# Kernel tuning notes

Measured on AMD Instinct MI355X. Metric: run time of the kernel, lower is better.

Reference implementation:

```python
import jax, jax.numpy as jnp
import numpy as np

C = 128      # c_in
H = 4        # no_heads
DH = 32      # c_hidden // no_heads (per-head dim)
INF = 1e9
EPS = 1e-5


def setup_inputs() -> dict:
    key = jax.random.key(0)
    ks = jax.random.split(key, 10)
    B, I, J = 1, 384, 384
    x = jax.random.normal(ks[0], (B, I, J, C), dtype=jnp.float32)
    mask = jnp.ones((B, I, J), dtype=jnp.float32)
    s = 0.02
    return {
        "x": x,
        "mask": mask,
        "ln_w": jnp.ones((C,), jnp.float32),
        "ln_b": jnp.zeros((C,), jnp.float32),
        "w_tri": jax.random.normal(ks[1], (C, H), jnp.float32) * s,   # bias=False
        "wq": jax.random.normal(ks[2], (C, H * DH), jnp.float32) * s,
        "wk": jax.random.normal(ks[3], (C, H * DH), jnp.float32) * s,
        "wv": jax.random.normal(ks[4], (C, H * DH), jnp.float32) * s,
        "wg": jax.random.normal(ks[5], (C, H * DH), jnp.float32) * s,
        "bg": jnp.zeros((H * DH,), jnp.float32),
        "wo": jax.random.normal(ks[6], (H * DH, C), jnp.float32) * s,
        "bo": jnp.zeros((C,), jnp.float32),
    }


def reference(x, mask, ln_w, ln_b, w_tri, wq, wk, wv, wg, bg, wo, bo):
    # starting=True: attend along rows (J axis), no transpose.
    B, I, J, _ = x.shape
    # LayerNorm over channel dim
    mu = jnp.mean(x, axis=-1, keepdims=True)
    var = jnp.mean(jnp.square(x - mu), axis=-1, keepdims=True)
    xn = (x - mu) * jax.lax.rsqrt(var + EPS) * ln_w + ln_b

    # mask bias: [B, I, 1, 1, J]
    mask_bias = (INF * (mask - 1.0))[:, :, None, None, :]
    # triangle bias: linear -> [B, I, J, H] -> permute (2,0,1) -> [B, H, I, J] -> [B, 1, H, I, J]
    tri = jnp.einsum('bijc,ch->bhij', xn, w_tri)[:, None]

    # multi-head attention with gating (OpenFold-style), batch dims (B, I), seq J
    q = jnp.einsum('bijc,cf->bijf', xn, wq).reshape(B, I, J, H, DH)
    k = jnp.einsum('bijc,cf->bijf', xn, wk).reshape(B, I, J, H, DH)
    v = jnp.einsum('bijc,cf->bijf', xn, wv).reshape(B, I, J, H, DH)
    q = q / np.sqrt(DH).astype(np.float32)

    # scores: [B, I, H, Q, K] + mask bias + triangle bias
    scores = jnp.einsum('biqhd,bikhd->bihqk', q, k) + mask_bias + tri
    a = jax.nn.softmax(scores, axis=-1)
    o = jnp.einsum('bihqk,bikhd->biqhd', a, v).reshape(B, I, J, H * DH)

    g = jax.nn.sigmoid(jnp.einsum('bijc,cf->bijf', xn, wg) + bg)
    o = o * g
    out = jnp.einsum('bijf,fc->bijc', o, wo) + bo
    return out
```

## Files before the change

### kernel.cpp

```cpp
#include <hip/hip_runtime.h>
#include <hip/hip_bf16.h>

#define NPOS (384*384)
#define JDIM 384
#define CDIM 128
#define HNUM 4
#define DHD  32

typedef __attribute__((ext_vector_type(8))) short short8;
typedef __attribute__((ext_vector_type(4))) float floatx4;
typedef unsigned short ushort_t;

__device__ __forceinline__ float bf2f(unsigned short u){
  unsigned int x = ((unsigned int)u) << 16;
  return __builtin_bit_cast(float, x);
}
__device__ __forceinline__ unsigned short f2bf(float f){
  unsigned int u = __builtin_bit_cast(unsigned int, f);
  u = u + 0x7FFFu + ((u >> 16) & 1u);
  return (unsigned short)(u >> 16);
}
__device__ __forceinline__ unsigned int pack2bf(float a, float b){
  unsigned int ua = __builtin_bit_cast(unsigned int, a);
  unsigned int ub = __builtin_bit_cast(unsigned int, b);
  ua = ua + 0x7FFFu + ((ua >> 16) & 1u);
  ub = ub + 0x7FFFu + ((ub >> 16) & 1u);
  return __builtin_amdgcn_perm(ub, ua, 0x07060302);
}

__global__ __launch_bounds__(256) void ln_tri_kernel(
    const float* __restrict__ x, const float* __restrict__ lnw,
    const float* __restrict__ lnb, const float* __restrict__ wtri,
    ushort_t* __restrict__ xn, float* __restrict__ trip)
{
  int wave = threadIdx.x >> 6, lane = threadIdx.x & 63;
  int pos = blockIdx.x * 4 + wave;
  const float2 xv = *(const float2*)(x + (size_t)pos*CDIM + lane*2);
  float x0 = xv.x, x1 = xv.y;
  float s = x0 + x1, ss = x0*x0 + x1*x1;
  #pragma unroll
  for (int o = 32; o > 0; o >>= 1){ s += __shfl_xor(s, o); ss += __shfl_xor(ss, o); }
  float mu  = s * (1.0f/128.0f);
  float var = ss * (1.0f/128.0f) - mu*mu;
  float rstd = rsqrtf(var + 1e-5f);
  float2 w2 = *(const float2*)(lnw + lane*2);
  float2 b2 = *(const float2*)(lnb + lane*2);
  float n0 = (x0 - mu)*rstd*w2.x + b2.x;
  float n1 = (x1 - mu)*rstd*w2.y + b2.y;
  ushort2 o2; o2.x = f2bf(n0); o2.y = f2bf(n1);
  *(ushort2*)(xn + (size_t)pos*CDIM + lane*2) = o2;
  float4 wt0 = *(const float4*)(wtri + lane*8);
  float4 wt1 = *(const float4*)(wtri + lane*8 + 4);
  float t0 = n0*wt0.x + n1*wt1.x;
  float t1 = n0*wt0.y + n1*wt1.y;
  float t2 = n0*wt0.z + n1*wt1.z;
  float t3 = n0*wt0.w + n1*wt1.w;
  #pragma unroll
  for (int o = 32; o > 0; o >>= 1){
    t0 += __shfl_xor(t0, o); t1 += __shfl_xor(t1, o);
    t2 += __shfl_xor(t2, o); t3 += __shfl_xor(t3, o);
  }
  if (lane == 0){
    trip[0*NPOS + pos] = t0;
    trip[1*NPOS + pos] = t1;
    trip[2*NPOS + pos] = t2;
    trip[3*NPOS + pos] = t3;
  }
}

__global__ __launch_bounds__(256) void wt_kernel(
    const float* wq, const float* wk, const float* wv,
    const float* wg, const float* wo, ushort_t* __restrict__ wt)
{
  int mat = blockIdx.x >> 6;
  int idx = ((blockIdx.x & 63) << 8) | threadIdx.x;
  const float* src = (mat==0)?wq:(mat==1)?wk:(mat==2)?wv:(mat==3)?wg:wo;
  int f = idx >> 7, c = idx & 127;
  wt[mat*16384 + idx] = f2bf(src[c*128 + f]);
}

__device__ __forceinline__ void gemm_body(
    const ushort_t* __restrict__ A, const ushort_t* __restrict__ W,
    void* __restrict__ outv, const float* __restrict__ bias,
    int mode, int row0, ushort_t* As, ushort_t* Bs)
{
  int t = threadIdx.x;
  #pragma unroll
  for (int i = 0; i < 8; i++){
    int v = t + i*256;
    int row = v >> 4, c8 = v & 15;
    *(short8*)(As + row*144 + c8*8) = *(const short8*)(A + (size_t)(row0+row)*CDIM + c8*8);
    *(short8*)(Bs + row*144 + c8*8) = *(const short8*)(W + v*8);
  }
  __syncthreads();
  int w = t >> 6, lane = t & 63;
  int wm = (w & 1) * 64, wn = (w >> 1) * 64;
  int m = lane & 15, q4 = lane >> 4;
  floatx4 acc[4][4];
  #pragma unroll
  for (int mi = 0; mi < 4; mi++)
    #pragma unroll
    for (int ni = 0; ni < 4; ni++)
      acc[mi][ni] = (floatx4){0.f, 0.f, 0.f, 0.f};
  #pragma unroll
  for (int k0 = 0; k0 < 128; k0 += 32){
    int koff = k0 + q4*8;
    short8 af[4], bf[4];
    #pragma unroll
    for (int mi = 0; mi < 4; mi++) af[mi] = *(const short8*)(As + (wm + mi*16 + m)*144 + koff);
    #pragma unroll
    for (int ni = 0; ni < 4; ni++) bf[ni] = *(const short8*)(Bs + (wn + ni*16 + m)*144 + koff);
    #pragma unroll
    for (int mi = 0; mi < 4; mi++)
      #pragma unroll
      for (int ni = 0; ni < 4; ni++)
        acc[mi][ni] = __builtin_amdgcn_mfma_f32_16x16x32_bf16(af[mi], bf[ni], acc[mi][ni], 0, 0, 0);
  }
  const float scale = 0.17677669529663687f;
  #pragma unroll
  for (int mi = 0; mi < 4; mi++){
    #pragma unroll
    for (int ni = 0; ni < 4; ni++){
      int col = wn + ni*16 + m;
      float bv = (mode >= 2) ? bias[col] : 0.f;
      #pragma unroll
      for (int r = 0; r < 4; r++){
        float val = acc[mi][ni][r];
        if (mode == 1) val *= scale;
        else if (mode == 2) val = 1.f / (1.f + __expf(-(val + bv)));
        else if (mode == 3) val += bv;
        int row = wm + mi*16 + q4*4 + r;
        size_t oidx = (size_t)(row0+row)*CDIM + col;
        if (mode == 3) ((float*)outv)[oidx] = val;
        else           ((ushort_t*)outv)[oidx] = f2bf(val);
      }
    }
  }
}

__global__ __launch_bounds__(256) void proj_gemm_kernel(
    const ushort_t* __restrict__ xn, const ushort_t* __restrict__ wt,
    ushort_t* __restrict__ outb, const float* __restrict__ bg)
{
  __shared__ __align__(16) ushort_t As[128*144];
  __shared__ __align__(16) ushort_t Bs[128*144];
  int proj = blockIdx.y;
  int mode = (proj == 0) ? 1 : (proj == 3) ? 2 : 0;
  gemm_body(xn, wt + proj*16384, outb + (size_t)proj*NPOS*CDIM, bg, mode,
            blockIdx.x * 128, As, Bs);
}

__global__ __launch_bounds__(256) void out_gemm_kernel(
    const ushort_t* __restrict__ og, const ushort_t* __restrict__ wt,
    float* __restrict__ out, const float* __restrict__ bo)
{
  __shared__ __align__(16) ushort_t As[128*144];
  __shared__ __align__(16) ushort_t Bs[128*144];
  gemm_body(og, wt, (void*)out, bo, 3, blockIdx.x * 128, As, Bs);
}

#define VT_STRIDE 392
#define P_STRIDE  40
__global__ __launch_bounds__(256, 2) void attn_kernel(
    const ushort_t* __restrict__ qb, const ushort_t* __restrict__ kb,
    const ushort_t* __restrict__ vb, const ushort_t* __restrict__ gb,
    const float* __restrict__ mask, const float* __restrict__ trip,
    ushort_t* __restrict__ og)
{
  __shared__ __align__(16) ushort_t Ks[JDIM*32];
  __shared__ __align__(16) ushort_t Vt[32*VT_STRIDE];
  __shared__ __align__(16) ushort_t Pb[4*96*P_STRIDE];
  int i = blockIdx.x, h = blockIdx.y;
  int t = threadIdx.x;
  size_t rbase = (size_t)i * JDIM;

  for (int idx = t; idx < JDIM*4; idx += 256){
    int j = idx >> 2, c8 = idx & 3;
    *(short8*)(Ks + j*32 + c8*8) = *(const short8*)(kb + (rbase + j)*CDIM + h*DHD + c8*8);
    short8 v8 = *(const short8*)(vb + (rbase + j)*CDIM + h*DHD + c8*8);
    int jb = j & 31;
    int jp = (j & ~31) | (((jb & 15) << 1) | (jb >> 4));
    #pragma unroll
    for (int e = 0; e < 8; e++) Vt[(c8*8 + e)*VT_STRIDE + jp] = (unsigned short)v8[e];
  }
  __syncthreads();

  int w = t >> 6, lane = t & 63;
  int m = lane & 15, q4 = lane >> 4;
  int wm = w * 96;
  ushort_t* Pw = Pb + w * 96 * P_STRIDE;

  short8 qf[6];
  #pragma unroll
  for (int t6 = 0; t6 < 6; t6++)
    qf[t6] = *(const short8*)(qb + (rbase + wm + t6*16 + m)*CDIM + h*DHD + q4*8);

  floatx4 oacc[6][2];
  float lpart[6][4];
  #pragma unroll
  for (int t6 = 0; t6 < 6; t6++){
    oacc[t6][0] = (floatx4){0.f,0.f,0.f,0.f};
    oacc[t6][1] = (floatx4){0.f,0.f,0.f,0.f};
    #pragma unroll
    for (int r = 0; r < 4; r++) lpart[t6][r] = 0.f;
  }

  const float* triph = trip + (size_t)h * NPOS;

  for (int kbk = 0; kbk < 12; kbk++){
    int col0 = kbk * 32;
    short8 kf0 = *(const short8*)(Ks + (col0 + m)*32 + q4*8);
    short8 kf1 = *(const short8*)(Ks + (col0 + 16 + m)*32 + q4*8);
    float mb0 = 1e9f * (mask[rbase + col0 + m] - 1.0f);
    float mb1 = 1e9f * (mask[rbase + col0 + 16 + m] - 1.0f);

    #pragma unroll
    for (int t6 = 0; t6 < 6; t6++){
      floatx4 z = (floatx4){0.f,0.f,0.f,0.f};
      floatx4 s0 = __builtin_amdgcn_mfma_f32_16x16x32_bf16(qf[t6], kf0, z, 0, 0, 0);
      floatx4 s1 = __builtin_amdgcn_mfma_f32_16x16x32_bf16(qf[t6], kf1, z, 0, 0, 0);
      int qrow = wm + t6*16 + q4*4;
      #pragma unroll
      for (int r = 0; r < 4; r++){
        const float* trow = triph + (size_t)(qrow + r)*JDIM + col0;
        float sc0 = s0[r] + mb0 + trow[m];
        float sc1 = s1[r] + mb1 + trow[16 + m];
        float p0 = __expf(sc0);
        float p1 = __expf(sc1);
        lpart[t6][r] += p0 + p1;
        *(unsigned int*)(Pw + (t6*16 + q4*4 + r)*P_STRIDE + m*2) = pack2bf(p0, p1);
      }
    }
    short8 vf0 = *(const short8*)(Vt + m*VT_STRIDE + col0 + q4*8);
    short8 vf1 = *(const short8*)(Vt + (16 + m)*VT_STRIDE + col0 + q4*8);
    #pragma unroll
    for (int t6 = 0; t6 < 6; t6++){
      short8 pf = *(const short8*)(Pw + (t6*16 + m)*P_STRIDE + q4*8);
      oacc[t6][0] = __builtin_amdgcn_mfma_f32_16x16x32_bf16(pf, vf0, oacc[t6][0], 0, 0, 0);
      oacc[t6][1] = __builtin_amdgcn_mfma_f32_16x16x32_bf16(pf, vf1, oacc[t6][1], 0, 0, 0);
    }
  }

  #pragma unroll
  for (int t6 = 0; t6 < 6; t6++)
    #pragma unroll
    for (int r = 0; r < 4; r++){
      float l = lpart[t6][r];
      l += __shfl_xor(l, 1); l += __shfl_xor(l, 2);
      l += __shfl_xor(l, 4); l += __shfl_xor(l, 8);
      lpart[t6][r] = 1.0f / (l + 1e-30f);
    }

  #pragma unroll
  for (int t6 = 0; t6 < 6; t6++){
    int qrow = wm + t6*16 + q4*4;
    #pragma unroll
    for (int dt = 0; dt < 2; dt++){
      #pragma unroll
      for (int r = 0; r < 4; r++){
        size_t oidx = (rbase + qrow + r)*CDIM + h*DHD + dt*16 + m;
        float o = oacc[t6][dt][r] * lpart[t6][r] * bf2f(gb[oidx]);
        og[oidx] = f2bf(o);
      }
    }
  }
}

extern "C" void kernel_launch(void* const* d_in, const int* in_sizes, int n_in,
                              void* d_out, int out_size, void* d_ws, size_t ws_size,
                              hipStream_t stream)
{
  const float* x    = (const float*)d_in[0];
  const float* mask = (const float*)d_in[1];
  const float* lnw  = (const float*)d_in[2];
  const float* lnb  = (const float*)d_in[3];
  const float* wtri = (const float*)d_in[4];
  const float* wq   = (const float*)d_in[5];
  const float* wk   = (const float*)d_in[6];
  const float* wv   = (const float*)d_in[7];
  const float* wg   = (const float*)d_in[8];
  const float* bg   = (const float*)d_in[9];
  const float* wo   = (const float*)d_in[10];
  const float* bo   = (const float*)d_in[11];

  char* ws = (char*)d_ws;
  const size_t SZ = (size_t)NPOS * CDIM * 2;
  ushort_t* xn  = (ushort_t*)(ws);
  ushort_t* qb  = (ushort_t*)(ws + 1*SZ);
  ushort_t* kbp = (ushort_t*)(ws + 2*SZ);
  ushort_t* vbp = (ushort_t*)(ws + 3*SZ);
  ushort_t* gbp = (ushort_t*)(ws + 4*SZ);
  ushort_t* og  = (ushort_t*)(ws + 5*SZ);
  ushort_t* wt  = (ushort_t*)(ws + 6*SZ);
  float*    tri = (float*)(ws + 6*SZ + 5*16384*2);

  ln_tri_kernel<<<NPOS/4, 256, 0, stream>>>(x, lnw, lnb, wtri, xn, tri);
  wt_kernel<<<320, 256, 0, stream>>>(wq, wk, wv, wg, wo, wt);
  proj_gemm_kernel<<<dim3(NPOS/128, 4), 256, 0, stream>>>(xn, wt, qb, bg);
  attn_kernel<<<dim3(JDIM, HNUM), 256, 0, stream>>>(qb, kbp, vbp, gbp, mask, tri, og);
  out_gemm_kernel<<<NPOS/128, 256, 0, stream>>>(og, wt + 4*16384, (float*)d_out, bo);
}
```

Before: 375.1 us.

## Fuse LayerNorm and triangle bias into projection GEMM; use exp2 and MFMA row sums

Removes the separate LayerNorm kernel. Each projection block now recomputes LayerNorm from the fp32 input directly into shared memory, which avoids writing and re-reading the bf16 normalized tensor. The triangle bias is written pre-scaled by log2e in a permuted column order, so the attention kernel can read it as float2 and use exp2. The softmax denominator now comes from an extra MFMA against a ones vector instead of shuffle reductions. In exchange, the fp32 input is read four times (once per projection), and the row sums are taken from bf16-rounded probabilities.

```diff
diff --git a/kernel.cpp b/kernel.cpp
--- a/kernel.cpp
+++ b/kernel.cpp
@@ -6,10 +6,20 @@
 #define CDIM 128
 #define HNUM 4
 #define DHD  32
+#define LOG2E 1.4426950408889634f
 
 typedef __attribute__((ext_vector_type(8))) short short8;
 typedef __attribute__((ext_vector_type(4))) float floatx4;
 typedef unsigned short ushort_t;
+
+#if defined(__has_builtin)
+#if __has_builtin(__builtin_amdgcn_exp2f)
+#define EXP2F(x) __builtin_amdgcn_exp2f(x)
+#endif
+#endif
+#ifndef EXP2F
+#define EXP2F(x) __expf((x) * 0.6931471805599453f)
+#endif
 
 __device__ __forceinline__ float bf2f(unsigned short u){
   unsigned int x = ((unsigned int)u) << 16;
@@ -28,46 +38,6 @@
   return __builtin_amdgcn_perm(ub, ua, 0x07060302);
 }
 
-__global__ __launch_bounds__(256) void ln_tri_kernel(
-    const float* __restrict__ x, const float* __restrict__ lnw,
-    const float* __restrict__ lnb, const float* __restrict__ wtri,
-    ushort_t* __restrict__ xn, float* __restrict__ trip)
-{
-  int wave = threadIdx.x >> 6, lane = threadIdx.x & 63;
-  int pos = blockIdx.x * 4 + wave;
-  const float2 xv = *(const float2*)(x + (size_t)pos*CDIM + lane*2);
-  float x0 = xv.x, x1 = xv.y;
-  float s = x0 + x1, ss = x0*x0 + x1*x1;
-  #pragma unroll
-  for (int o = 32; o > 0; o >>= 1){ s += __shfl_xor(s, o); ss += __shfl_xor(ss, o); }
-  float mu  = s * (1.0f/128.0f);
-  float var = ss * (1.0f/128.0f) - mu*mu;
-  float rstd = rsqrtf(var + 1e-5f);
-  float2 w2 = *(const float2*)(lnw + lane*2);
-  float2 b2 = *(const float2*)(lnb + lane*2);
-  float n0 = (x0 - mu)*rstd*w2.x + b2.x;
-  float n1 = (x1 - mu)*rstd*w2.y + b2.y;
-  ushort2 o2; o2.x = f2bf(n0); o2.y = f2bf(n1);
-  *(ushort2*)(xn + (size_t)pos*CDIM + lane*2) = o2;
-  float4 wt0 = *(const float4*)(wtri + lane*8);
-  float4 wt1 = *(const float4*)(wtri + lane*8 + 4);
-  float t0 = n0*wt0.x + n1*wt1.x;
-  float t1 = n0*wt0.y + n1*wt1.y;
-  float t2 = n0*wt0.z + n1*wt1.z;
-  float t3 = n0*wt0.w + n1*wt1.w;
-  #pragma unroll
-  for (int o = 32; o > 0; o >>= 1){
-    t0 += __shfl_xor(t0, o); t1 += __shfl_xor(t1, o);
-    t2 += __shfl_xor(t2, o); t3 += __shfl_xor(t3, o);
-  }
-  if (lane == 0){
-    trip[0*NPOS + pos] = t0;
-    trip[1*NPOS + pos] = t1;
-    trip[2*NPOS + pos] = t2;
-    trip[3*NPOS + pos] = t3;
-  }
-}
-
 __global__ __launch_bounds__(256) void wt_kernel(
     const float* wq, const float* wk, const float* wv,
     const float* wg, const float* wo, ushort_t* __restrict__ wt)
@@ -79,18 +49,137 @@
   wt[mat*16384 + idx] = f2bf(src[c*128 + f]);
 }
 
-__device__ __forceinline__ void gemm_body(
-    const ushort_t* __restrict__ A, const ushort_t* __restrict__ W,
-    void* __restrict__ outv, const float* __restrict__ bias,
-    int mode, int row0, ushort_t* As, ushort_t* Bs)
-{
+__global__ __launch_bounds__(256, 2) void proj_fused_kernel(
+    const float* __restrict__ x, const float* __restrict__ lnw,
+    const float* __restrict__ lnb, const float* __restrict__ wtri,
+    const ushort_t* __restrict__ wt, ushort_t* __restrict__ outb,
+    const float* __restrict__ bg, float* __restrict__ trip2)
+{
+  __shared__ __align__(16) ushort_t As[128*144];
+  __shared__ __align__(16) ushort_t Bs[128*144];
   int t = threadIdx.x;
+  int proj = blockIdx.y;
+  int row0 = blockIdx.x * 128;
+  ushort_t* outp = outb + (size_t)proj * NPOS * CDIM;
+
+  const ushort_t* W = wt + proj*16384;
   #pragma unroll
   for (int i = 0; i < 8; i++){
     int v = t + i*256;
     int row = v >> 4, c8 = v & 15;
-    *(short8*)(As + row*144 + c8*8) = *(const short8*)(A + (size_t)(row0+row)*CDIM + c8*8);
     *(short8*)(Bs + row*144 + c8*8) = *(const short8*)(W + v*8);
+  }
+
+  int row = t >> 1, ch0 = (t & 1) * 64;
+  const float* xr = x + (size_t)(row0 + row)*CDIM + ch0;
+  float xv[64];
+  float s = 0.f, ss = 0.f;
+  #pragma unroll
+  for (int c4 = 0; c4 < 16; c4++){
+    float4 f4 = *(const float4*)(xr + c4*4);
+    xv[c4*4+0]=f4.x; xv[c4*4+1]=f4.y; xv[c4*4+2]=f4.z; xv[c4*4+3]=f4.w;
+    s += f4.x+f4.y+f4.z+f4.w;
+    ss += f4.x*f4.x+f4.y*f4.y+f4.z*f4.z+f4.w*f4.w;
+  }
+  s += __shfl_xor(s, 1); ss += __shfl_xor(ss, 1);
+  float mu = s*(1.0f/128.0f);
+  float var = ss*(1.0f/128.0f) - mu*mu;
+  float rstd = rsqrtf(var + 1e-5f);
+  float t0=0.f, t1=0.f, t2=0.f, t3=0.f;
+  #pragma unroll
+  for (int c4 = 0; c4 < 16; c4++){
+    float4 w4 = *(const float4*)(lnw + ch0 + c4*4);
+    float4 b4 = *(const float4*)(lnb + ch0 + c4*4);
+    float n0 = (xv[c4*4+0]-mu)*rstd*w4.x + b4.x;
+    float n1 = (xv[c4*4+1]-mu)*rstd*w4.y + b4.y;
+    float n2 = (xv[c4*4+2]-mu)*rstd*w4.z + b4.z;
+    float n3 = (xv[c4*4+3]-mu)*rstd*w4.w + b4.w;
+    ushort4 o4; o4.x=f2bf(n0); o4.y=f2bf(n1); o4.z=f2bf(n2); o4.w=f2bf(n3);
+    *(ushort4*)(As + row*144 + ch0 + c4*4) = o4;
+    if (proj == 0){
+      const float* wtb = wtri + (ch0 + c4*4)*4;
+      float4 wt0 = *(const float4*)(wtb);
+      float4 wt1 = *(const float4*)(wtb + 4);
+      float4 wt2 = *(const float4*)(wtb + 8);
+      float4 wt3 = *(const float4*)(wtb + 12);
+      t0 += n0*wt0.x + n1*wt1.x + n2*wt2.x + n3*wt3.x;
+      t1 += n0*wt0.y + n1*wt1.y + n2*wt2.y + n3*wt3.y;
+      t2 += n0*wt0.z + n1*wt1.z + n2*wt2.z + n3*wt3.z;
+      t3 += n0*wt0.w + n1*wt1.w + n2*wt2.w + n3*wt3.w;
+    }
+  }
+  if (proj == 0){
+    t0 += __shfl_xor(t0,1); t1 += __shfl_xor(t1,1);
+    t2 += __shfl_xor(t2,1); t3 += __shfl_xor(t3,1);
+    if ((t & 1) == 0){
+      int p = row0 + row;
+      int ii = p / JDIM, j = p - ii*JDIM;
+      int jp = (j & ~31) | ((j & 15) << 1) | ((j & 31) >> 4);
+      size_t base = (size_t)ii*JDIM + jp;
+      trip2[0*NPOS + base] = t0 * LOG2E;
+      trip2[1*NPOS + base] = t1 * LOG2E;
+      trip2[2*NPOS + base] = t2 * LOG2E;
+      trip2[3*NPOS + base] = t3 * LOG2E;
+    }
+  }
+  __syncthreads();
+
+  int w = t >> 6, lane = t & 63;
+  int wm = (w & 1) * 64, wn = (w >> 1) * 64;
+  int m = lane & 15, q4 = lane >> 4;
+  floatx4 acc[4][4];
+  #pragma unroll
+  for (int mi = 0; mi < 4; mi++)
+    #pragma unroll
+    for (int ni = 0; ni < 4; ni++)
+      acc[mi][ni] = (floatx4){0.f, 0.f, 0.f, 0.f};
+  #pragma unroll
+  for (int k0 = 0; k0 < 128; k0 += 32){
+    int koff = k0 + q4*8;
+    short8 af[4], bf[4];
+    #pragma unroll
+    for (int mi = 0; mi < 4; mi++) af[mi] = *(const short8*)(As + (wm + mi*16 + m)*144 + koff);
+    #pragma unroll
+    for (int ni = 0; ni < 4; ni++) bf[ni] = *(const short8*)(Bs + (wn + ni*16 + m)*144 + koff);
+    #pragma unroll
+    for (int mi = 0; mi < 4; mi++)
+      #pragma unroll
+      for (int ni = 0; ni < 4; ni++)
+        acc[mi][ni] = __builtin_amdgcn_mfma_f32_16x16x32_bf16(af[mi], bf[ni], acc[mi][ni], 0, 0, 0);
+  }
+  const float qscale = 0.17677669529663687f * LOG2E;
+  #pragma unroll
+  for (int mi = 0; mi < 4; mi++){
+    #pragma unroll
+    for (int ni = 0; ni < 4; ni++){
+      int col = wn + ni*16 + m;
+      float bv = (proj == 3) ? bg[col] : 0.f;
+      #pragma unroll
+      for (int r = 0; r < 4; r++){
+        float val = acc[mi][ni][r];
+        if (proj == 0) val *= qscale;
+        else if (proj == 3) val = 1.f / (1.f + __expf(-(val + bv)));
+        int orow = wm + mi*16 + q4*4 + r;
+        outp[(size_t)(row0+orow)*CDIM + col] = f2bf(val);
+      }
+    }
+  }
+}
+
+__global__ __launch_bounds__(256) void out_gemm_kernel(
+    const ushort_t* __restrict__ og, const ushort_t* __restrict__ wt,
+    float* __restrict__ out, const float* __restrict__ bo)
+{
+  __shared__ __align__(16) ushort_t As[128*144];
+  __shared__ __align__(16) ushort_t Bs[128*144];
+  int t = threadIdx.x;
+  int row0 = blockIdx.x * 128;
+  #pragma unroll
+  for (int i = 0; i < 8; i++){
+    int v = t + i*256;
+    int row = v >> 4, c8 = v & 15;
+    *(short8*)(As + row*144 + c8*8) = *(const short8*)(og + (size_t)(row0+row)*CDIM + c8*8);
+    *(short8*)(Bs + row*144 + c8*8) = *(const short8*)(wt + v*8);
   }
   __syncthreads();
   int w = t >> 6, lane = t & 63;
@@ -116,47 +205,18 @@
       for (int ni = 0; ni < 4; ni++)
         acc[mi][ni] = __builtin_amdgcn_mfma_f32_16x16x32_bf16(af[mi], bf[ni], acc[mi][ni], 0, 0, 0);
   }
-  const float scale = 0.17677669529663687f;
-  #pragma unroll
-  for (int mi = 0; mi < 4; mi++){
+  #pragma unroll
+  for (int mi = 0; mi < 4; mi++)
     #pragma unroll
     for (int ni = 0; ni < 4; ni++){
       int col = wn + ni*16 + m;
-      float bv = (mode >= 2) ? bias[col] : 0.f;
+      float bv = bo[col];
       #pragma unroll
       for (int r = 0; r < 4; r++){
-        float val = acc[mi][ni][r];
-        if (mode == 1) val *= scale;
-        else if (mode == 2) val = 1.f / (1.f + __expf(-(val + bv)));
-        else if (mode == 3) val += bv;
-        int row = wm + mi*16 + q4*4 + r;
-        size_t oidx = (size_t)(row0+row)*CDIM + col;
-        if (mode == 3) ((float*)outv)[oidx] = val;
-        else           ((ushort_t*)outv)[oidx] = f2bf(val);
+        int orow = wm + mi*16 + q4*4 + r;
+        out[(size_t)(row0+orow)*CDIM + col] = acc[mi][ni][r] + bv;
       }
     }
-  }
-}
-
-__global__ __launch_bounds__(256) void proj_gemm_kernel(
-    const ushort_t* __restrict__ xn, const ushort_t* __restrict__ wt,
-    ushort_t* __restrict__ outb, const float* __restrict__ bg)
-{
-  __shared__ __align__(16) ushort_t As[128*144];
-  __shared__ __align__(16) ushort_t Bs[128*144];
-  int proj = blockIdx.y;
-  int mode = (proj == 0) ? 1 : (proj == 3) ? 2 : 0;
-  gemm_body(xn, wt + proj*16384, outb + (size_t)proj*NPOS*CDIM, bg, mode,
-            blockIdx.x * 128, As, Bs);
-}
-
-__global__ __launch_bounds__(256) void out_gemm_kernel(
-    const ushort_t* __restrict__ og, const ushort_t* __restrict__ wt,
-    float* __restrict__ out, const float* __restrict__ bo)
-{
-  __shared__ __align__(16) ushort_t As[128*144];
-  __shared__ __align__(16) ushort_t Bs[128*144];
-  gemm_body(og, wt, (void*)out, bo, 3, blockIdx.x * 128, As, Bs);
 }
 
 #define VT_STRIDE 392
@@ -164,7 +224,7 @@
 __global__ __launch_bounds__(256, 2) void attn_kernel(
     const ushort_t* __restrict__ qb, const ushort_t* __restrict__ kb,
     const ushort_t* __restrict__ vb, const ushort_t* __restrict__ gb,
-    const float* __restrict__ mask, const float* __restrict__ trip,
+    const float* __restrict__ mask, const float* __restrict__ trip2,
     ushort_t* __restrict__ og)
 {
   __shared__ __align__(16) ushort_t Ks[JDIM*32];
@@ -195,24 +255,24 @@
   for (int t6 = 0; t6 < 6; t6++)
     qf[t6] = *(const short8*)(qb + (rbase + wm + t6*16 + m)*CDIM + h*DHD + q4*8);
 
+  const short8 ones = (short8){0x3F80,0x3F80,0x3F80,0x3F80,0x3F80,0x3F80,0x3F80,0x3F80};
   floatx4 oacc[6][2];
-  float lpart[6][4];
+  floatx4 lacc[6];
   #pragma unroll
   for (int t6 = 0; t6 < 6; t6++){
     oacc[t6][0] = (floatx4){0.f,0.f,0.f,0.f};
     oacc[t6][1] = (floatx4){0.f,0.f,0.f,0.f};
-    #pragma unroll
-    for (int r = 0; r < 4; r++) lpart[t6][r] = 0.f;
-  }
-
-  const float* triph = trip + (size_t)h * NPOS;
+    lacc[t6]    = (floatx4){0.f,0.f,0.f,0.f};
+  }
+
+  const float* triph = trip2 + (size_t)h * NPOS;
 
   for (int kbk = 0; kbk < 12; kbk++){
     int col0 = kbk * 32;
     short8 kf0 = *(const short8*)(Ks + (col0 + m)*32 + q4*8);
     short8 kf1 = *(const short8*)(Ks + (col0 + 16 + m)*32 + q4*8);
-    float mb0 = 1e9f * (mask[rbase + col0 + m] - 1.0f);
-    float mb1 = 1e9f * (mask[rbase + col0 + 16 + m] - 1.0f);
+    float mb0 = (1e9f*LOG2E) * (mask[rbase + col0 + m] - 1.0f);
+    float mb1 = (1e9f*LOG2E) * (mask[rbase + col0 + 16 + m] - 1.0f);
 
     #pragma unroll
     for (int t6 = 0; t6 < 6; t6++){
@@ -220,14 +280,12 @@
       floatx4 s0 = __builtin_amdgcn_mfma_f32_16x16x32_bf16(qf[t6], kf0, z, 0, 0, 0);
       floatx4 s1 = __builtin_amdgcn_mfma_f32_16x16x32_bf16(qf[t6], kf1, z, 0, 0, 0);
       int qrow = wm + t6*16 + q4*4;
+      const float* trow = triph + (size_t)qrow*JDIM + col0 + m*2;
       #pragma unroll
       for (int r = 0; r < 4; r++){
-        const float* trow = triph + (size_t)(qrow + r)*JDIM + col0;
-        float sc0 = s0[r] + mb0 + trow[m];
-        float sc1 = s1[r] + mb1 + trow[16 + m];
-        float p0 = __expf(sc0);
-        float p1 = __expf(sc1);
-        lpart[t6][r] += p0 + p1;
+        float2 t2 = *(const float2*)(trow + r*JDIM);
+        float p0 = EXP2F(s0[r] + mb0 + t2.x);
+        float p1 = EXP2F(s1[r] + mb1 + t2.y);
         *(unsigned int*)(Pw + (t6*16 + q4*4 + r)*P_STRIDE + m*2) = pack2bf(p0, p1);
       }
     }
@@ -238,28 +296,20 @@
       short8 pf = *(const short8*)(Pw + (t6*16 + m)*P_STRIDE + q4*8);
       oacc[t6][0] = __builtin_amdgcn_mfma_f32_16x16x32_bf16(pf, vf0, oacc[t6][0], 0, 0, 0);
       oacc[t6][1] = __builtin_amdgcn_mfma_f32_16x16x32_bf16(pf, vf1, oacc[t6][1], 0, 0, 0);
-    }
-  }
-
-  #pragma unroll
-  for (int t6 = 0; t6 < 6; t6++)
-    #pragma unroll
-    for (int r = 0; r < 4; r++){
-      float l = lpart[t6][r];
-      l += __shfl_xor(l, 1); l += __shfl_xor(l, 2);
-      l += __shfl_xor(l, 4); l += __shfl_xor(l, 8);
-      lpart[t6][r] = 1.0f / (l + 1e-30f);
-    }
+      lacc[t6]    = __builtin_amdgcn_mfma_f32_16x16x32_bf16(pf, ones, lacc[t6], 0, 0, 0);
+    }
+  }
 
   #pragma unroll
   for (int t6 = 0; t6 < 6; t6++){
     int qrow = wm + t6*16 + q4*4;
     #pragma unroll
-    for (int dt = 0; dt < 2; dt++){
-      #pragma unroll
-      for (int r = 0; r < 4; r++){
+    for (int r = 0; r < 4; r++){
+      float rl = 1.0f / (lacc[t6][r] + 1e-30f);
+      #pragma unroll
+      for (int dt = 0; dt < 2; dt++){
         size_t oidx = (rbase + qrow + r)*CDIM + h*DHD + dt*16 + m;
-        float o = oacc[t6][dt][r] * lpart[t6][r] * bf2f(gb[oidx]);
+        float o = oacc[t6][dt][r] * rl * bf2f(gb[oidx]);
         og[oidx] = f2bf(o);
       }
     }
@@ -285,18 +335,17 @@
 
   char* ws = (char*)d_ws;
   const size_t SZ = (size_t)NPOS * CDIM * 2;
-  ushort_t* xn  = (ushort_t*)(ws);
-  ushort_t* qb  = (ushort_t*)(ws + 1*SZ);
-  ushort_t* kbp = (ushort_t*)(ws + 2*SZ);
-  ushort_t* vbp = (ushort_t*)(ws + 3*SZ);
-  ushort_t* gbp = (ushort_t*)(ws + 4*SZ);
-  ushort_t* og  = (ushort_t*)(ws + 5*SZ);
-  ushort_t* wt  = (ushort_t*)(ws + 6*SZ);
-  float*    tri = (float*)(ws + 6*SZ + 5*16384*2);
-
-  ln_tri_kernel<<<NPOS/4, 256, 0, stream>>>(x, lnw, lnb, wtri, xn, tri);
+  ushort_t* qb  = (ushort_t*)(ws);
+  ushort_t* kbp = (ushort_t*)(ws + 1*SZ);
+  ushort_t* vbp = (ushort_t*)(ws + 2*SZ);
+  ushort_t* gbp = (ushort_t*)(ws + 3*SZ);
+  ushort_t* og  = (ushort_t*)(ws + 4*SZ);
+  ushort_t* wt  = (ushort_t*)(ws + 5*SZ);
+  float*    tri = (float*)(ws + 5*SZ + 5*16384*2);
+
   wt_kernel<<<320, 256, 0, stream>>>(wq, wk, wv, wg, wo, wt);
-  proj_gemm_kernel<<<dim3(NPOS/128, 4), 256, 0, stream>>>(xn, wt, qb, bg);
+  proj_fused_kernel<<<dim3(NPOS/128, 4), 256, 0, stream>>>(
+      x, lnw, lnb, wtri, wt, qb, bg, tri);
   attn_kernel<<<dim3(JDIM, HNUM), 256, 0, stream>>>(qb, kbp, vbp, gbp, mask, tri, og);
   out_gemm_kernel<<<NPOS/128, 256, 0, stream>>>(og, wt + 4*16384, (float*)d_out, bo);
 }
```

Measured after the change: 407.7 us. 8.7% more time.
